# Optimization experiments

Measured on AMD Instinct MI355X. Metric: run time of the kernel, lower is better.

The kernel has to match this reference:

```python
import jax, jax.numpy as jnp
import numpy as np

B, N, M, C = 8, 2048, 2048, 512


def setup_inputs() -> dict:
    key = jax.random.key(0)
    ks = jax.random.split(key, 10)
    s = 1.0 / np.sqrt(C)
    dec_embed = jax.random.normal(ks[0], (B, N, C), dtype=jnp.float32)
    enc_embed = jax.random.normal(ks[1], (B, M, C), dtype=jnp.float32)
    trans_mat = (jax.random.uniform(ks[2], (B, N, M)) < 0.5).astype(jnp.float32)
    Wv = jax.random.uniform(ks[3], (C, C), minval=-s, maxval=s, dtype=jnp.float32)
    bv = jax.random.uniform(ks[4], (C,), minval=-s, maxval=s, dtype=jnp.float32)
    W1 = jax.random.uniform(ks[5], (C, C), minval=-s, maxval=s, dtype=jnp.float32)
    b1 = jax.random.uniform(ks[6], (C,), minval=-s, maxval=s, dtype=jnp.float32)
    W2 = jax.random.uniform(ks[7], (C, C), minval=-s, maxval=s, dtype=jnp.float32)
    b2 = jax.random.uniform(ks[8], (C,), minval=-s, maxval=s, dtype=jnp.float32)
    return {"dec_embed": dec_embed, "enc_embed": enc_embed, "trans_mat": trans_mat,
            "Wv": Wv, "bv": bv, "W1": W1, "b1": b1, "W2": W2, "b2": b2}


def reference(dec_embed, enc_embed, trans_mat, Wv, bv, W1, b1, W2, b2):
    # scores [B,N,M], elementwise-masked by trans_mat
    attn = jnp.einsum('bnc,bmc->bnm', dec_embed, enc_embed) * trans_mat
    # NONSTANDARD masked softmax: zeros participate in softmax (exp(0)=1 in denom),
    # then positions where attn==0 are re-zeroed.
    sm = jax.nn.softmax(attn, axis=-1)
    attn = jnp.where(attn != 0, sm, jnp.zeros((), attn.dtype))
    v = enc_embed @ Wv + bv                      # [B,M,C]
    v = jnp.tanh(jnp.einsum('bnm,bmc->bnc', attn, v))  # [B,N,C]
    g = dec_embed * v + dec_embed                # tanh-gate + residual
    h = jax.nn.relu(g @ W1 + b1)                 # Mlp fc1 + ReLU (drop=0)
    return h @ W2 + b2                           # Mlp fc2
```

## Files before the change

kernel.cpp:

```cpp
#include <hip/hip_runtime.h>
#include <math.h>

#define Bb 8
#define Nn 2048
#define Mm 2048
#define Cc 512

typedef __attribute__((ext_vector_type(8))) _Float16 hfrag;
typedef __attribute__((ext_vector_type(4))) float f4;
typedef __attribute__((ext_vector_type(4))) _Float16 h4;

__device__ __forceinline__ void gld16(const void* g, void* l) {
    __builtin_amdgcn_global_load_lds(
        (const __attribute__((address_space(1))) void*)g,
        (__attribute__((address_space(3))) void*)l, 16, 0, 0);
}

template<int N> __device__ __forceinline__ void wait_vmcnt() {
    if constexpr (N == 0)      asm volatile("s_waitcnt vmcnt(0)" ::: "memory");
    else if constexpr (N == 3) asm volatile("s_waitcnt vmcnt(3)" ::: "memory");
    else if constexpr (N == 4) asm volatile("s_waitcnt vmcnt(4)" ::: "memory");
    __builtin_amdgcn_sched_barrier(0);
}

template<int EPI, int BN, int SWZ>
__global__ __launch_bounds__(256) void gemm_mfma(
    const _Float16* __restrict__ Ah, long sA, int lda,
    const _Float16* __restrict__ Bh, long sB, int ldb,
    const float* __restrict__ aux, long sAux, int ldaux,
    const _Float16* __restrict__ aux2,
    float* __restrict__ mlal,
    void* __restrict__ Cout, long sC, int ldc, int K, int GX)
{
    constexpr int NI  = (BN == 128) ? 4 : 2;
    constexpr int ASL = 512;
    constexpr int BSL = BN * 4;
    constexpr int NQ  = (ASL + BSL) / 256;

    __shared__ _Float16 As[3][128 * 32];
    __shared__ _Float16 Bs[3][BN * 32];
    __shared__ _Float16 AlS[(EPI == 2) ? 32 * 128 : 4];

    int bx, by, bz;
    if (SWZ == 1) {
        const int id = blockIdx.x;
        bz = id & 7; bx = (id >> 3) % GX; by = (id >> 3) / GX;
    } else if (SWZ == 2) {
        const int id = blockIdx.x;
        bz = 0; bx = (id >> 3) % GX; by = (id & 7) + 8 * ((id >> 3) / GX);
    } else {
        bx = blockIdx.x; by = blockIdx.y; bz = 0;
    }

    const _Float16* A0 = Ah + (size_t)bz * sA;
    const _Float16* B0 = Bh + (size_t)bz * sB;

    const int tid  = threadIdx.x;
    const int wv   = tid >> 6;
    const int ln   = tid & 63;
    const int wx   = (BN == 128) ? (wv & 1) : 0;
    const int wy   = (BN == 128) ? (wv >> 1) : wv;
    const int lcol = ln & 15, quad = ln >> 4;
    const int row0w = wy * (NI * 16);
    const int col0w = wx * 64;

    const int rowBase = by * 128;
    const int colBase = bx * BN;

    const int soff = (quad ^ ((lcol >> 1) & 3)) * 8;

    f4 acc[NI][4];
    const f4 z4 = {0.f, 0.f, 0.f, 0.f};
    #pragma unroll
    for (int i = 0; i < NI; ++i)
        #pragma unroll
        for (int j = 0; j < 4; ++j) acc[i][j] = z4;

    if (EPI == 2) {
        const float* alb = mlal + (size_t)bz * (2048 * 32);
        #pragma unroll
        for (int q = 0; q < 16; ++q) {
            const int idx = q * 256 + tid;
            const int col = idx >> 5, tt = idx & 31;
            AlS[tt * 128 + col] = (_Float16)alb[(size_t)(colBase + col) * 32 + tt];
        }
        asm volatile("s_waitcnt lgkmcnt(0)" ::: "memory");
        __builtin_amdgcn_sched_barrier(0);
    }
    _Float16 als[4] = {(_Float16)0.f, (_Float16)0.f, (_Float16)0.f, (_Float16)0.f};

    auto STAGE = [&](int k0, int p) {
        #pragma unroll
        for (int q = 0; q < NQ; ++q) {
            const int c = q * 256 + wv * 64 + ln;
            if (c < ASL) {
                const int r = c >> 2;
                const int g = (c & 3) ^ ((c >> 3) & 3);
                gld16(A0 + (size_t)(rowBase + r) * lda + k0 + g * 8, &As[p][c * 8]);
            } else {
                const int cb = c - ASL;
                const int r  = cb >> 2;
                const int g  = (cb & 3) ^ ((cb >> 3) & 3);
                gld16(B0 + (size_t)(colBase + r) * ldb + k0 + g * 8, &Bs[p][cb * 8]);
            }
        }
    };

    const int NT = K >> 5;
    STAGE(0, 0);
    STAGE(32, 1);
    wait_vmcnt<NQ>();
    __builtin_amdgcn_s_barrier();

    int p = 0, pn2 = 2;
    for (int t = 0; t < NT; ++t) {
        if (t + 2 < NT) STAGE((t + 2) * 32, pn2);

        if (EPI == 2 && (t & 1) == 0) {
            const int tt = t >> 1;
            #pragma unroll
            for (int j = 0; j < 4; ++j)
                als[j] = AlS[tt * 128 + col0w + j * 16 + lcol];
        }

        hfrag af[NI], bf_[4];
        #pragma unroll
        for (int i = 0; i < NI; ++i)
            af[i]  = *(const hfrag*)&As[p][(row0w + i * 16 + lcol) * 32 + soff];
        #pragma unroll
        for (int j = 0; j < 4; ++j)
            bf_[j] = *(const hfrag*)&Bs[p][(col0w + j * 16 + lcol) * 32 + soff];

        if (EPI == 2) {
            #pragma unroll
            for (int j = 0; j < 4; ++j) bf_[j] = bf_[j] * als[j];
        }

        #pragma unroll
        for (int i = 0; i < NI; ++i)
            #pragma unroll
            for (int j = 0; j < 4; ++j)
                acc[i][j] = __builtin_amdgcn_mfma_f32_16x16x32_f16(af[i], bf_[j], acc[i][j], 0, 0, 0);

        if (t + 1 < NT) {
            if (t + 2 < NT) wait_vmcnt<NQ>();
            else            wait_vmcnt<0>();
            __builtin_amdgcn_s_barrier();
        }
        p   = (p   == 2) ? 0 : p + 1;
        pn2 = (pn2 == 2) ? 0 : pn2 + 1;
    }

    const int crow0 = rowBase + row0w + quad * 4;
    const int ccol0 = colBase + col0w + lcol;

    if (EPI == 0) {
        _Float16* E = (_Float16*)Cout + (size_t)bz * sC;
        const float* Mk = aux + (size_t)bz * sAux;
        const int t = (rowBase + row0w) >> 6;

        f4 mkA[NI], mkB[NI];
        #pragma unroll
        for (int i = 0; i < NI; ++i)
            mkA[i] = *(const f4*)(Mk + (size_t)ccol0 * ldaux + crow0 + i * 16);
        #pragma unroll
        for (int i = 0; i < NI; ++i)
            mkB[i] = *(const f4*)(Mk + (size_t)(ccol0 + 16) * ldaux + crow0 + i * 16);

        #pragma unroll
        for (int j = 0; j < 4; ++j) {
            const int n = ccol0 + j * 16;
            f4 mkN[NI];
            if (j < 2) {
                #pragma unroll
                for (int i = 0; i < NI; ++i)
                    mkN[i] = *(const f4*)(Mk + (size_t)(n + 32) * ldaux + crow0 + i * 16);
            }
            #pragma unroll
            for (int i = 0; i < NI; ++i)
                #pragma unroll
                for (int r = 0; r < 4; ++r) acc[i][j][r] *= mkA[i][r];

            float mx = acc[0][j][0];
            #pragma unroll
            for (int i = 0; i < NI; ++i)
                #pragma unroll
                for (int r = 0; r < 4; ++r) mx = fmaxf(mx, acc[i][j][r]);
            mx = fmaxf(mx, __shfl_xor(mx, 16, 64));
            mx = fmaxf(mx, __shfl_xor(mx, 32, 64));
            float l0 = 0.f;
            #pragma unroll
            for (int i = 0; i < NI; ++i) {
                h4 ev;
                #pragma unroll
                for (int r = 0; r < 4; ++r) {
                    const float s = acc[i][j][r];
                    const float e = __expf(s - mx);
                    l0 += e;
                    ev[r] = (s == 0.f) ? (_Float16)0.f : (_Float16)e;
                }
                *(h4*)(E + (size_t)n * ldc + crow0 + i * 16) = ev;
            }
            l0 += __shfl_xor(l0, 16, 64);
            l0 += __shfl_xor(l0, 32, 64);
            if (quad == 0) {
                float2 pq; pq.x = mx; pq.y = l0;
                ((float2*)mlal)[((size_t)bz * 2048 + n) * 32 + t] = pq;
            }
            #pragma unroll
            for (int i = 0; i < NI; ++i) { mkA[i] = mkB[i]; }
            if (j < 2) {
                #pragma unroll
                for (int i = 0; i < NI; ++i) mkB[i] = mkN[i];
            }
        }
    } else if (EPI == 1) {
        _Float16* C = (_Float16*)Cout;
        #pragma unroll
        for (int j = 0; j < 4; ++j) {
            const int col = ccol0 + j * 16;
            const float bi = aux[col];
            #pragma unroll
            for (int i = 0; i < NI; ++i) {
                const int rowb = crow0 + i * 16;
                const int bb = rowb >> 11, ml = rowb & 2047;
                h4 st;
                #pragma unroll
                for (int r = 0; r < 4; ++r) st[r] = (_Float16)(acc[i][j][r] + bi);
                *(h4*)(C + (size_t)bb * ((size_t)Cc * Mm) + (size_t)col * Mm + ml) = st;
            }
        }
    } else if (EPI == 2) {
        _Float16* C = (_Float16*)Cout + (size_t)bz * sC;
        const _Float16* Dg = aux2 + (size_t)bz * sC;
        #pragma unroll
        for (int i = 0; i < NI; ++i) {
            const int c0 = crow0 + i * 16;
            #pragma unroll
            for (int j = 0; j < 4; ++j) {
                const int n = ccol0 + j * 16;
                const h4 dv = *(const h4*)(Dg + (size_t)n * ldc + c0);
                h4 gv;
                #pragma unroll
                for (int r = 0; r < 4; ++r) {
                    const float a = acc[i][j][r];
                    const float th = 1.f - 2.f / (__expf(2.f * a) + 1.f);
                    gv[r] = (_Float16)((float)dv[r] * (1.f + th));
                }
                *(h4*)(C + (size_t)n * ldc + c0) = gv;
            }
        }
    } else if (EPI == 3) {
        _Float16* C = (_Float16*)Cout;
        #pragma unroll
        for (int i = 0; i < NI; ++i) {
            const int c0 = crow0 + i * 16;
            const f4 bi = *(const f4*)(aux + c0);
            #pragma unroll
            for (int j = 0; j < 4; ++j) {
                const int n = ccol0 + j * 16;
                h4 hv;
                #pragma unroll
                for (int r = 0; r < 4; ++r)
                    hv[r] = (_Float16)fmaxf(acc[i][j][r] + bi[r], 0.f);
                *(h4*)(C + (size_t)n * ldc + c0) = hv;
            }
        }
    } else {
        float* C = (float*)Cout;
        #pragma unroll
        for (int i = 0; i < NI; ++i) {
            const int c0 = crow0 + i * 16;
            const f4 bi = *(const f4*)(aux + c0);
            #pragma unroll
            for (int j = 0; j < 4; ++j) {
                const int n = ccol0 + j * 16;
                f4 ov;
                #pragma unroll
                for (int r = 0; r < 4; ++r) ov[r] = acc[i][j][r] + bi[r];
                *(f4*)(C + (size_t)n * ldc + c0) = ov;
            }
        }
    }
}

__global__ __launch_bounds__(64) void combine_kernel(
    const float* __restrict__ mlq, float* __restrict__ alpha)
{
    const int row = blockIdx.x * 64 + threadIdx.x;
    const float2* ml = (const float2*)mlq + (size_t)row * 32;
    float mt[32], lt[32];
    float m = -1e30f;
    #pragma unroll
    for (int t = 0; t < 32; ++t) {
        float2 p = ml[t];
        mt[t] = p.x; lt[t] = p.y;
        m = fmaxf(m, p.x);
    }
    float et[32], l = 0.f;
    #pragma unroll
    for (int t = 0; t < 32; ++t) {
        et[t] = __expf(mt[t] - m);
        l += lt[t] * et[t];
    }
    const float inv = 1.f / l;
    float* ap = alpha + (size_t)row * 32;
    #pragma unroll
    for (int t = 0; t < 32; ++t) ap[t] = et[t] * inv;
}

__global__ __launch_bounds__(256) void sconv(const float* __restrict__ x,
                                             _Float16* __restrict__ o)
{
    const size_t i = (size_t)blockIdx.x * 256 + threadIdx.x;
    f4 v = ((const f4*)x)[i];
    h4 hh;
    #pragma unroll
    for (int k = 0; k < 4; ++k) hh[k] = (_Float16)v[k];
    ((h4*)o)[i] = hh;
}

__global__ __launch_bounds__(256) void wconv(const float* s0, const float* s1, const float* s2,
                                             _Float16* d0, _Float16* d1, _Float16* d2)
{
    const float* Sm = blockIdx.z == 0 ? s0 : blockIdx.z == 1 ? s1 : s2;
    _Float16* D = blockIdx.z == 0 ? d0 : blockIdx.z == 1 ? d1 : d2;
    __shared__ float t[32][33];
    const int x = threadIdx.x & 31, y = threadIdx.x >> 5;
    const int gx = blockIdx.x * 32, gy = blockIdx.y * 32;
    #pragma unroll
    for (int yy = y; yy < 32; yy += 8)
        t[yy][x] = Sm[(size_t)(gy + yy) * 512 + gx + x];
    __syncthreads();
    #pragma unroll
    for (int yy = y; yy < 32; yy += 8)
        D[(size_t)(gx + yy) * 512 + gy + x] = (_Float16)t[x][yy];
}

extern "C" void kernel_launch(void* const* d_in, const int* in_sizes, int n_in,
                              void* d_out, int out_size, void* d_ws, size_t ws_size,
                              hipStream_t stream)
{
    const float* dec   = (const float*)d_in[0];
    const float* enc   = (const float*)d_in[1];
    const float* trans = (const float*)d_in[2];
    const float* Wv = (const float*)d_in[3];
    const float* bv = (const float*)d_in[4];
    const float* W1 = (const float*)d_in[5];
    const float* b1 = (const float*)d_in[6];
    const float* W2 = (const float*)d_in[7];
    const float* b2 = (const float*)d_in[8];

    char* ws = (char*)d_ws;
    _Float16* e     = (_Float16*)ws;
    float*    mlq   = (float*)(ws + 0x4000000);
    float*    alpha = (float*)(ws + 0x4400000);
    _Float16* dec_h = (_Float16*)(ws + 0x4600000);
    _Float16* Wvt   = (_Float16*)(ws + 0x5600000);
    _Float16* W1t   = Wvt + 262144;
    _Float16* W2t   = Wvt + 524288;
    _Float16* vT    = (_Float16*)(ws + 0x5800000);
    _Float16* g     = (_Float16*)(ws + 0x6800000);
    _Float16* h     = (_Float16*)(ws + 0x7800000);
    _Float16* enc_h = (_Float16*)d_out;

    sconv<<<dim3(8192), 256, 0, stream>>>(dec, dec_h);
    sconv<<<dim3(8192), 256, 0, stream>>>(enc, enc_h);
    wconv<<<dim3(16, 16, 3), 256, 0, stream>>>(Wv, W1, W2, Wvt, W1t, W2t);

    gemm_mfma<0, 128, 1><<<dim3(2048), 256, 0, stream>>>(
        enc_h, (long)Mm * Cc, 512,
        dec_h, (long)Nn * Cc, 512,
        trans, (long)Nn * Mm, 2048, nullptr, mlq,
        e, (long)Nn * Mm, 2048, 512, 16);

    combine_kernel<<<dim3(256), 64, 0, stream>>>(mlq, alpha);

    gemm_mfma<1, 64, 2><<<dim3(1024), 256, 0, stream>>>(
        enc_h, 0, 512, Wvt, 0, 512, bv, 0, 0, nullptr, nullptr,
        vT, 0, 0, 512, 8);

    gemm_mfma<2, 128, 1><<<dim3(512), 256, 0, stream>>>(
        vT, (long)Cc * Mm, 2048,
        e, (long)Nn * Mm, 2048,
        nullptr, 0, 512, dec_h, alpha,
        g, (long)Nn * Cc, 512, 2048, 16);

    gemm_mfma<3, 64, 0><<<dim3(256, 4), 256, 0, stream>>>(
        W1t, 0, 512, g, 0, 512, b1, 0, 0, nullptr, nullptr,
        h, 0, 512, 512, 0);

    gemm_mfma<4, 64, 0><<<dim3(256, 4), 256, 0, stream>>>(
        W2t, 0, 512, h, 0, 512, b2, 0, 0, nullptr, nullptr,
        d_out, 0, 512, 512, 0);
}
```

Measured before the change: 444.8 us.

## Use dedicated 256x256-tile, 512-thread kernel for masked score GEMM

Replaces the score GEMM (EPI 0 of the generic kernel, 128x128 tiles with 256 threads) with a dedicated kernel using 256x256 tiles, 8 waves, and 8x4 MFMA accumulators per wave. Larger tiles double operand reuse from LDS and cut global load traffic per FLOP. The masked-softmax epilogue still writes per-64-row partial max/sum entries so the combine step is unchanged. In exchange it uses much more LDS (96KB triple-buffered) and registers, giving lower occupancy and only 512 blocks.

```diff
diff --git a/kernel.cpp b/kernel.cpp
--- a/kernel.cpp
+++ b/kernel.cpp
@@ -21,6 +21,153 @@
     else if constexpr (N == 3) asm volatile("s_waitcnt vmcnt(3)" ::: "memory");
     else if constexpr (N == 4) asm volatile("s_waitcnt vmcnt(4)" ::: "memory");
     __builtin_amdgcn_sched_barrier(0);
+}
+
+__global__ __launch_bounds__(512) void score256(
+    const _Float16* __restrict__ Ah, long sA, int lda,
+    const _Float16* __restrict__ Bh, long sB, int ldb,
+    const float* __restrict__ Mk0, long sAux, int ldaux,
+    float* __restrict__ mlq,
+    _Float16* __restrict__ E, long sC, int ldc, int K, int GX)
+{
+    constexpr int NQ = 4;
+    __shared__ _Float16 As[3][256 * 32];
+    __shared__ _Float16 Bs[3][256 * 32];
+
+    const int id = blockIdx.x;
+    const int bz = id & 7;
+    const int bx = (id >> 3) % GX;
+    const int by = (id >> 3) / GX;
+
+    const _Float16* A0 = Ah + (size_t)bz * sA;
+    const _Float16* B0 = Bh + (size_t)bz * sB;
+
+    const int tid  = threadIdx.x;
+    const int wv   = tid >> 6;
+    const int ln   = tid & 63;
+    const int lcol = ln & 15, quad = ln >> 4;
+    const int row0w = (wv >> 2) * 128;
+    const int col0w = (wv & 3) * 64;
+    const int rowBase = by * 256;
+    const int colBase = bx * 256;
+    const int soff = (quad ^ ((lcol >> 1) & 3)) * 8;
+
+    f4 acc[8][4];
+    const f4 z4 = {0.f, 0.f, 0.f, 0.f};
+    #pragma unroll
+    for (int i = 0; i < 8; ++i)
+        #pragma unroll
+        for (int j = 0; j < 4; ++j) acc[i][j] = z4;
+
+    auto STAGE = [&](int k0, int p) {
+        #pragma unroll
+        for (int q = 0; q < 4; ++q) {
+            const int c = q * 512 + tid;
+            if (c < 1024) {
+                const int r = c >> 2;
+                const int g = (c & 3) ^ ((c >> 3) & 3);
+                gld16(A0 + (size_t)(rowBase + r) * lda + k0 + g * 8, &As[p][c * 8]);
+            } else {
+                const int cb = c - 1024;
+                const int r  = cb >> 2;
+                const int g  = (cb & 3) ^ ((cb >> 3) & 3);
+                gld16(B0 + (size_t)(colBase + r) * ldb + k0 + g * 8, &Bs[p][cb * 8]);
+            }
+        }
+    };
+
+    const int NT = K >> 5;
+    STAGE(0, 0);
+    STAGE(32, 1);
+    wait_vmcnt<NQ>();
+    __builtin_amdgcn_s_barrier();
+
+    int p = 0, pn2 = 2;
+    for (int t = 0; t < NT; ++t) {
+        if (t + 2 < NT) STAGE((t + 2) * 32, pn2);
+
+        hfrag af[8], bf_[4];
+        #pragma unroll
+        for (int i = 0; i < 8; ++i)
+            af[i]  = *(const hfrag*)&As[p][(row0w + i * 16 + lcol) * 32 + soff];
+        #pragma unroll
+        for (int j = 0; j < 4; ++j)
+            bf_[j] = *(const hfrag*)&Bs[p][(col0w + j * 16 + lcol) * 32 + soff];
+
+        #pragma unroll
+        for (int i = 0; i < 8; ++i)
+            #pragma unroll
+            for (int j = 0; j < 4; ++j)
+                acc[i][j] = __builtin_amdgcn_mfma_f32_16x16x32_f16(af[i], bf_[j], acc[i][j], 0, 0, 0);
+
+        if (t + 1 < NT) {
+            if (t + 2 < NT) wait_vmcnt<NQ>();
+            else            wait_vmcnt<0>();
+            __builtin_amdgcn_s_barrier();
+        }
+        p   = (p   == 2) ? 0 : p + 1;
+        pn2 = (pn2 == 2) ? 0 : pn2 + 1;
+    }
+
+    const int crow0 = rowBase + row0w + quad * 4;
+    const int ccol0 = colBase + col0w + lcol;
+    const int t0 = (rowBase + row0w) >> 6;
+    _Float16* Eb = E + (size_t)bz * sC;
+    const float* Mk = Mk0 + (size_t)bz * sAux;
+
+    f4 mk[8], mkN[8];
+    #pragma unroll
+    for (int i = 0; i < 8; ++i)
+        mk[i] = *(const f4*)(Mk + (size_t)ccol0 * ldaux + crow0 + i * 16);
+
+    #pragma unroll
+    for (int j = 0; j < 4; ++j) {
+        const int n = ccol0 + j * 16;
+        if (j < 3) {
+            #pragma unroll
+            for (int i = 0; i < 8; ++i)
+                mkN[i] = *(const f4*)(Mk + (size_t)(n + 16) * ldaux + crow0 + i * 16);
+        }
+        #pragma unroll
+        for (int i = 0; i < 8; ++i)
+            #pragma unroll
+            for (int r = 0; r < 4; ++r) acc[i][j][r] *= mk[i][r];
+
+        #pragma unroll
+        for (int cch = 0; cch < 2; ++cch) {
+            const int ib = cch * 4;
+            float mx = acc[ib][j][0];
+            #pragma unroll
+            for (int i = 0; i < 4; ++i)
+                #pragma unroll
+                for (int r = 0; r < 4; ++r) mx = fmaxf(mx, acc[ib + i][j][r]);
+            mx = fmaxf(mx, __shfl_xor(mx, 16, 64));
+            mx = fmaxf(mx, __shfl_xor(mx, 32, 64));
+            float l0 = 0.f;
+            #pragma unroll
+            for (int i = 0; i < 4; ++i) {
+                h4 ev;
+                #pragma unroll
+                for (int r = 0; r < 4; ++r) {
+                    const float s = acc[ib + i][j][r];
+                    const float e = __expf(s - mx);
+                    l0 += e;
+                    ev[r] = (s == 0.f) ? (_Float16)0.f : (_Float16)e;
+                }
+                *(h4*)(Eb + (size_t)n * ldc + crow0 + (ib + i) * 16) = ev;
+            }
+            l0 += __shfl_xor(l0, 16, 64);
+            l0 += __shfl_xor(l0, 32, 64);
+            if (quad == 0) {
+                float2 pq; pq.x = mx; pq.y = l0;
+                ((float2*)mlq)[((size_t)bz * 2048 + n) * 32 + t0 + cch] = pq;
+            }
+        }
+        if (j < 3) {
+            #pragma unroll
+            for (int i = 0; i < 8; ++i) mk[i] = mkN[i];
+        }
+    }
 }
 
 template<int EPI, int BN, int SWZ>
@@ -154,67 +301,7 @@
     const int crow0 = rowBase + row0w + quad * 4;
     const int ccol0 = colBase + col0w + lcol;
 
-    if (EPI == 0) {
-        _Float16* E = (_Float16*)Cout + (size_t)bz * sC;
-        const float* Mk = aux + (size_t)bz * sAux;
-        const int t = (rowBase + row0w) >> 6;
-
-        f4 mkA[NI], mkB[NI];
-        #pragma unroll
-        for (int i = 0; i < NI; ++i)
-            mkA[i] = *(const f4*)(Mk + (size_t)ccol0 * ldaux + crow0 + i * 16);
-        #pragma unroll
-        for (int i = 0; i < NI; ++i)
-            mkB[i] = *(const f4*)(Mk + (size_t)(ccol0 + 16) * ldaux + crow0 + i * 16);
-
-        #pragma unroll
-        for (int j = 0; j < 4; ++j) {
-            const int n = ccol0 + j * 16;
-            f4 mkN[NI];
-            if (j < 2) {
-                #pragma unroll
-                for (int i = 0; i < NI; ++i)
-                    mkN[i] = *(const f4*)(Mk + (size_t)(n + 32) * ldaux + crow0 + i * 16);
-            }
-            #pragma unroll
-            for (int i = 0; i < NI; ++i)
-                #pragma unroll
-                for (int r = 0; r < 4; ++r) acc[i][j][r] *= mkA[i][r];
-
-            float mx = acc[0][j][0];
-            #pragma unroll
-            for (int i = 0; i < NI; ++i)
-                #pragma unroll
-                for (int r = 0; r < 4; ++r) mx = fmaxf(mx, acc[i][j][r]);
-            mx = fmaxf(mx, __shfl_xor(mx, 16, 64));
-            mx = fmaxf(mx, __shfl_xor(mx, 32, 64));
-            float l0 = 0.f;
-            #pragma unroll
-            for (int i = 0; i < NI; ++i) {
-                h4 ev;
-                #pragma unroll
-                for (int r = 0; r < 4; ++r) {
-                    const float s = acc[i][j][r];
-                    const float e = __expf(s - mx);
-                    l0 += e;
-                    ev[r] = (s == 0.f) ? (_Float16)0.f : (_Float16)e;
-                }
-                *(h4*)(E + (size_t)n * ldc + crow0 + i * 16) = ev;
-            }
-            l0 += __shfl_xor(l0, 16, 64);
-            l0 += __shfl_xor(l0, 32, 64);
-            if (quad == 0) {
-                float2 pq; pq.x = mx; pq.y = l0;
-                ((float2*)mlal)[((size_t)bz * 2048 + n) * 32 + t] = pq;
-            }
-            #pragma unroll
-            for (int i = 0; i < NI; ++i) { mkA[i] = mkB[i]; }
-            if (j < 2) {
-                #pragma unroll
-                for (int i = 0; i < NI; ++i) mkB[i] = mkN[i];
-            }
-        }
-    } else if (EPI == 1) {
+    if (EPI == 1) {
         _Float16* C = (_Float16*)Cout;
         #pragma unroll
         for (int j = 0; j < 4; ++j) {
@@ -368,11 +455,11 @@
     sconv<<<dim3(8192), 256, 0, stream>>>(enc, enc_h);
     wconv<<<dim3(16, 16, 3), 256, 0, stream>>>(Wv, W1, W2, Wvt, W1t, W2t);
 
-    gemm_mfma<0, 128, 1><<<dim3(2048), 256, 0, stream>>>(
+    score256<<<dim3(512), 512, 0, stream>>>(
         enc_h, (long)Mm * Cc, 512,
         dec_h, (long)Nn * Cc, 512,
-        trans, (long)Nn * Mm, 2048, nullptr, mlq,
-        e, (long)Nn * Mm, 2048, 512, 16);
+        trans, (long)Nn * Mm, 2048, mlq,
+        e, (long)Nn * Mm, 2048, 512, 8);
 
     combine_kernel<<<dim3(256), 64, 0, stream>>>(mlq, alpha);
 
```

Measured after the change: 439.6 us. Within noise of the previous version (-1.2%).

## Fuse masked-score, softmax and PV GEMM into one flash-style attention kernel

Applied to the files above, without the earlier changes.

Replaces the score GEMM with its masked-exp epilogue, the combine kernel and the alpha-scaled PV GEMM with a single kernel. The new kernel keeps a running max and sum per row over 256-wide M tiles and stages the probability tile in LDS. It then feeds that tile straight into the PV MFMAs and applies the tanh gate in the epilogue. This avoids writing and re-reading the large fp16 score matrix and the per-tile max/sum buffers, and drops two launches. In exchange it runs one 256-thread block per CU with heavy LDS use, several barriers per tile and only double buffering, so latency may be poorly hidden.

```diff
diff --git a/kernel.cpp b/kernel.cpp
--- a/kernel.cpp
+++ b/kernel.cpp
@@ -23,13 +23,222 @@
     __builtin_amdgcn_sched_barrier(0);
 }
 
+__global__ __launch_bounds__(256, 1) void attn_fused(
+    const _Float16* __restrict__ Eg,
+    const _Float16* __restrict__ Qg,
+    const _Float16* __restrict__ Vg,
+    const float*    __restrict__ Mg,
+    _Float16* __restrict__ Gg)
+{
+    __shared__ _Float16 EA[2][256 * 32];
+    __shared__ _Float16 QB[2][64 * 32];
+    __shared__ _Float16 VA[2][512 * 32];
+    __shared__ _Float16 PL[64 * 256];
+    __shared__ float MXS[4][64];
+    __shared__ float LSS[4][64];
+
+    const int id = blockIdx.x;
+    const int bz = id & 7;
+    const int n0 = (id >> 3) * 64;
+
+    const _Float16* E0 = Eg + (size_t)bz * ((size_t)Mm * Cc);
+    const _Float16* Q0 = Qg + (size_t)bz * ((size_t)Nn * Cc) + (size_t)n0 * Cc;
+    const _Float16* V0 = Vg + (size_t)bz * ((size_t)Cc * Mm);
+    const float*    M0 = Mg + (size_t)bz * ((size_t)Nn * Mm);
+
+    const int tid = threadIdx.x;
+    const int wv = tid >> 6, ln = tid & 63;
+    const int lcol = ln & 15, quad = ln >> 4;
+    const int soff = (quad ^ ((lcol >> 1) & 3)) * 8;
+    char* PLb = (char*)PL;
+
+    f4 o[8][4];
+    const f4 z4 = {0.f, 0.f, 0.f, 0.f};
+    #pragma unroll
+    for (int i = 0; i < 8; ++i)
+        #pragma unroll
+        for (int j = 0; j < 4; ++j) o[i][j] = z4;
+    float mrun[4] = {0.f, 0.f, 0.f, 0.f};
+    float lrun[4] = {0.f, 0.f, 0.f, 0.f};
+
+    for (int mt = 0; mt < 8; ++mt) {
+        const int m0 = mt * 256;
+
+        f4 sa[4][4];
+        #pragma unroll
+        for (int i = 0; i < 4; ++i)
+            #pragma unroll
+            for (int j = 0; j < 4; ++j) sa[i][j] = z4;
+
+        auto SSTAGE = [&](int k0, int p) {
+            #pragma unroll
+            for (int q = 0; q < 5; ++q) {
+                const int c = q * 256 + tid;
+                if (c < 1024) {
+                    const int r = c >> 2, gsw = (c & 3) ^ ((c >> 3) & 3);
+                    gld16(E0 + (size_t)(m0 + r) * Cc + k0 + gsw * 8, &EA[p][c * 8]);
+                } else {
+                    const int cb = c - 1024;
+                    const int r = cb >> 2, gsw = (cb & 3) ^ ((cb >> 3) & 3);
+                    gld16(Q0 + (size_t)r * Cc + k0 + gsw * 8, &QB[p][cb * 8]);
+                }
+            }
+        };
+        const float* Mkb = M0 + (size_t)(n0 + lcol) * Mm + m0 + wv * 64 + quad * 4;
+        f4 mk[4], mkN[4];
+        #pragma unroll
+        for (int i = 0; i < 4; ++i) mk[i] = *(const f4*)(Mkb + i * 16);
+
+        SSTAGE(0, 0);
+        __syncthreads();
+        for (int t = 0; t < 16; ++t) {
+            const int p = t & 1;
+            if (t + 1 < 16) SSTAGE((t + 1) * 32, p ^ 1);
+            hfrag af[4], bf[4];
+            #pragma unroll
+            for (int i = 0; i < 4; ++i)
+                af[i] = *(const hfrag*)&EA[p][(wv * 64 + i * 16 + lcol) * 32 + soff];
+            #pragma unroll
+            for (int j = 0; j < 4; ++j)
+                bf[j] = *(const hfrag*)&QB[p][(j * 16 + lcol) * 32 + soff];
+            #pragma unroll
+            for (int i = 0; i < 4; ++i)
+                #pragma unroll
+                for (int j = 0; j < 4; ++j)
+                    sa[i][j] = __builtin_amdgcn_mfma_f32_16x16x32_f16(af[i], bf[j], sa[i][j], 0, 0, 0);
+            if (t + 1 < 16) __syncthreads();
+        }
+
+        #pragma unroll
+        for (int j = 0; j < 4; ++j) {
+            if (j < 3) {
+                #pragma unroll
+                for (int i = 0; i < 4; ++i)
+                    mkN[i] = *(const f4*)(Mkb + (size_t)(j + 1) * 16 * Mm + i * 16);
+            }
+            #pragma unroll
+            for (int i = 0; i < 4; ++i)
+                #pragma unroll
+                for (int r = 0; r < 4; ++r) sa[i][j][r] *= mk[i][r];
+            float mx = 0.f;
+            #pragma unroll
+            for (int i = 0; i < 4; ++i)
+                #pragma unroll
+                for (int r = 0; r < 4; ++r) mx = fmaxf(mx, sa[i][j][r]);
+            mx = fmaxf(mx, __shfl_xor(mx, 16, 64));
+            mx = fmaxf(mx, __shfl_xor(mx, 32, 64));
+            if (quad == 0) MXS[wv][j * 16 + lcol] = mx;
+            if (j < 3) {
+                #pragma unroll
+                for (int i = 0; i < 4; ++i) mk[i] = mkN[i];
+            }
+        }
+        __syncthreads();
+
+        float al[4], mnew[4];
+        #pragma unroll
+        for (int j = 0; j < 4; ++j) {
+            const int n = j * 16 + lcol;
+            float mm = mrun[j];
+            mm = fmaxf(mm, MXS[0][n]); mm = fmaxf(mm, MXS[1][n]);
+            mm = fmaxf(mm, MXS[2][n]); mm = fmaxf(mm, MXS[3][n]);
+            al[j] = __expf(mrun[j] - mm);
+            mrun[j] = mm; mnew[j] = mm;
+        }
+        #pragma unroll
+        for (int j = 0; j < 4; ++j) {
+            const int n = j * 16 + lcol;
+            float lp = 0.f;
+            #pragma unroll
+            for (int i = 0; i < 4; ++i) {
+                h4 pv;
+                #pragma unroll
+                for (int r = 0; r < 4; ++r) {
+                    const float s = sa[i][j][r];
+                    const float e = __expf(s - mnew[j]);
+                    lp += e;
+                    pv[r] = (s == 0.f) ? (_Float16)0.f : (_Float16)e;
+                }
+                *(h4*)(PLb + n * 512 +
+                       (((wv << 7) + (i << 5) + (quad << 3)) ^ ((n & 7) << 4))) = pv;
+            }
+            lp += __shfl_xor(lp, 16, 64);
+            lp += __shfl_xor(lp, 32, 64);
+            if (quad == 0) LSS[wv][n] = lp;
+        }
+        __syncthreads();
+
+        #pragma unroll
+        for (int j = 0; j < 4; ++j) {
+            const int n = j * 16 + lcol;
+            const float ls = LSS[0][n] + LSS[1][n] + LSS[2][n] + LSS[3][n];
+            lrun[j] = lrun[j] * al[j] + ls;
+            #pragma unroll
+            for (int i = 0; i < 8; ++i)
+                #pragma unroll
+                for (int r = 0; r < 4; ++r) o[i][j][r] *= al[j];
+        }
+
+        auto VSTAGE = [&](int k0, int p) {
+            #pragma unroll
+            for (int q = 0; q < 8; ++q) {
+                const int c = q * 256 + tid;
+                const int r = c >> 2, gsw = (c & 3) ^ ((c >> 3) & 3);
+                gld16(V0 + (size_t)r * Mm + m0 + k0 + gsw * 8, &VA[p][c * 8]);
+            }
+        };
+        VSTAGE(0, 0);
+        __syncthreads();
+        for (int t = 0; t < 8; ++t) {
+            const int p = t & 1;
+            if (t + 1 < 8) VSTAGE((t + 1) * 32, p ^ 1);
+            hfrag va[8], pb[4];
+            #pragma unroll
+            for (int i = 0; i < 8; ++i)
+                va[i] = *(const hfrag*)&VA[p][(wv * 128 + i * 16 + lcol) * 32 + soff];
+            #pragma unroll
+            for (int j = 0; j < 4; ++j) {
+                const int n = j * 16 + lcol;
+                pb[j] = *(const hfrag*)(PLb + n * 512 +
+                        (((t << 6) + (quad << 4)) ^ ((n & 7) << 4)));
+            }
+            #pragma unroll
+            for (int i = 0; i < 8; ++i)
+                #pragma unroll
+                for (int j = 0; j < 4; ++j)
+                    o[i][j] = __builtin_amdgcn_mfma_f32_16x16x32_f16(va[i], pb[j], o[i][j], 0, 0, 0);
+            if (t + 1 < 8) __syncthreads();
+        }
+        __syncthreads();
+    }
+
+    const _Float16* Db = Qg + (size_t)bz * ((size_t)Nn * Cc);
+    _Float16* Gb = Gg + (size_t)bz * ((size_t)Nn * Cc);
+    #pragma unroll
+    for (int j = 0; j < 4; ++j) {
+        const int n = n0 + j * 16 + lcol;
+        const float inv = 1.f / lrun[j];
+        #pragma unroll
+        for (int i = 0; i < 8; ++i) {
+            const int c0 = wv * 128 + i * 16 + quad * 4;
+            const h4 dv = *(const h4*)(Db + (size_t)n * Cc + c0);
+            h4 gv;
+            #pragma unroll
+            for (int r = 0; r < 4; ++r) {
+                const float a = o[i][j][r] * inv;
+                const float th = 1.f - 2.f / (__expf(2.f * a) + 1.f);
+                gv[r] = (_Float16)((float)dv[r] * (1.f + th));
+            }
+            *(h4*)(Gb + (size_t)n * Cc + c0) = gv;
+        }
+    }
+}
+
 template<int EPI, int BN, int SWZ>
 __global__ __launch_bounds__(256) void gemm_mfma(
     const _Float16* __restrict__ Ah, long sA, int lda,
     const _Float16* __restrict__ Bh, long sB, int ldb,
     const float* __restrict__ aux, long sAux, int ldaux,
-    const _Float16* __restrict__ aux2,
-    float* __restrict__ mlal,
     void* __restrict__ Cout, long sC, int ldc, int K, int GX)
 {
     constexpr int NI  = (BN == 128) ? 4 : 2;
@@ -39,7 +248,6 @@
 
     __shared__ _Float16 As[3][128 * 32];
     __shared__ _Float16 Bs[3][BN * 32];
-    __shared__ _Float16 AlS[(EPI == 2) ? 32 * 128 : 4];
 
     int bx, by, bz;
     if (SWZ == 1) {
@@ -66,7 +274,6 @@
 
     const int rowBase = by * 128;
     const int colBase = bx * BN;
-
     const int soff = (quad ^ ((lcol >> 1) & 3)) * 8;
 
     f4 acc[NI][4];
@@ -75,19 +282,6 @@
     for (int i = 0; i < NI; ++i)
         #pragma unroll
         for (int j = 0; j < 4; ++j) acc[i][j] = z4;
-
-    if (EPI == 2) {
-        const float* alb = mlal + (size_t)bz * (2048 * 32);
-        #pragma unroll
-        for (int q = 0; q < 16; ++q) {
-            const int idx = q * 256 + tid;
-            const int col = idx >> 5, tt = idx & 31;
-            AlS[tt * 128 + col] = (_Float16)alb[(size_t)(colBase + col) * 32 + tt];
-        }
-        asm volatile("s_waitcnt lgkmcnt(0)" ::: "memory");
-        __builtin_amdgcn_sched_barrier(0);
-    }
-    _Float16 als[4] = {(_Float16)0.f, (_Float16)0.f, (_Float16)0.f, (_Float16)0.f};
 
     auto STAGE = [&](int k0, int p) {
         #pragma unroll
@@ -116,13 +310,6 @@
     for (int t = 0; t < NT; ++t) {
         if (t + 2 < NT) STAGE((t + 2) * 32, pn2);
 
-        if (EPI == 2 && (t & 1) == 0) {
-            const int tt = t >> 1;
-            #pragma unroll
-            for (int j = 0; j < 4; ++j)
-                als[j] = AlS[tt * 128 + col0w + j * 16 + lcol];
-        }
-
         hfrag af[NI], bf_[4];
         #pragma unroll
         for (int i = 0; i < NI; ++i)
@@ -130,11 +317,6 @@
         #pragma unroll
         for (int j = 0; j < 4; ++j)
             bf_[j] = *(const hfrag*)&Bs[p][(col0w + j * 16 + lcol) * 32 + soff];
-
-        if (EPI == 2) {
-            #pragma unroll
-            for (int j = 0; j < 4; ++j) bf_[j] = bf_[j] * als[j];
-        }
 
         #pragma unroll
         for (int i = 0; i < NI; ++i)
@@ -154,67 +336,7 @@
     const int crow0 = rowBase + row0w + quad * 4;
     const int ccol0 = colBase + col0w + lcol;
 
-    if (EPI == 0) {
-        _Float16* E = (_Float16*)Cout + (size_t)bz * sC;
-        const float* Mk = aux + (size_t)bz * sAux;
-        const int t = (rowBase + row0w) >> 6;
-
-        f4 mkA[NI], mkB[NI];
-        #pragma unroll
-        for (int i = 0; i < NI; ++i)
-            mkA[i] = *(const f4*)(Mk + (size_t)ccol0 * ldaux + crow0 + i * 16);
-        #pragma unroll
-        for (int i = 0; i < NI; ++i)
-            mkB[i] = *(const f4*)(Mk + (size_t)(ccol0 + 16) * ldaux + crow0 + i * 16);
-
-        #pragma unroll
-        for (int j = 0; j < 4; ++j) {
-            const int n = ccol0 + j * 16;
-            f4 mkN[NI];
-            if (j < 2) {
-                #pragma unroll
-                for (int i = 0; i < NI; ++i)
-                    mkN[i] = *(const f4*)(Mk + (size_t)(n + 32) * ldaux + crow0 + i * 16);
-            }
-            #pragma unroll
-            for (int i = 0; i < NI; ++i)
-                #pragma unroll
-                for (int r = 0; r < 4; ++r) acc[i][j][r] *= mkA[i][r];
-
-            float mx = acc[0][j][0];
-            #pragma unroll
-            for (int i = 0; i < NI; ++i)
-                #pragma unroll
-                for (int r = 0; r < 4; ++r) mx = fmaxf(mx, acc[i][j][r]);
-            mx = fmaxf(mx, __shfl_xor(mx, 16, 64));
-            mx = fmaxf(mx, __shfl_xor(mx, 32, 64));
-            float l0 = 0.f;
-            #pragma unroll
-            for (int i = 0; i < NI; ++i) {
-                h4 ev;
-                #pragma unroll
-                for (int r = 0; r < 4; ++r) {
-                    const float s = acc[i][j][r];
-                    const float e = __expf(s - mx);
-                    l0 += e;
-                    ev[r] = (s == 0.f) ? (_Float16)0.f : (_Float16)e;
-                }
-                *(h4*)(E + (size_t)n * ldc + crow0 + i * 16) = ev;
-            }
-            l0 += __shfl_xor(l0, 16, 64);
-            l0 += __shfl_xor(l0, 32, 64);
-            if (quad == 0) {
-                float2 pq; pq.x = mx; pq.y = l0;
-                ((float2*)mlal)[((size_t)bz * 2048 + n) * 32 + t] = pq;
-            }
-            #pragma unroll
-            for (int i = 0; i < NI; ++i) { mkA[i] = mkB[i]; }
-            if (j < 2) {
-                #pragma unroll
-                for (int i = 0; i < NI; ++i) mkB[i] = mkN[i];
-            }
-        }
-    } else if (EPI == 1) {
+    if (EPI == 1) {
         _Float16* C = (_Float16*)Cout;
         #pragma unroll
         for (int j = 0; j < 4; ++j) {
@@ -230,26 +352,6 @@
                 *(h4*)(C + (size_t)bb * ((size_t)Cc * Mm) + (size_t)col * Mm + ml) = st;
             }
         }
-    } else if (EPI == 2) {
-        _Float16* C = (_Float16*)Cout + (size_t)bz * sC;
-        const _Float16* Dg = aux2 + (size_t)bz * sC;
-        #pragma unroll
-        for (int i = 0; i < NI; ++i) {
-            const int c0 = crow0 + i * 16;
-            #pragma unroll
-            for (int j = 0; j < 4; ++j) {
-                const int n = ccol0 + j * 16;
-                const h4 dv = *(const h4*)(Dg + (size_t)n * ldc + c0);
-                h4 gv;
-                #pragma unroll
-                for (int r = 0; r < 4; ++r) {
-                    const float a = acc[i][j][r];
-                    const float th = 1.f - 2.f / (__expf(2.f * a) + 1.f);
-                    gv[r] = (_Float16)((float)dv[r] * (1.f + th));
-                }
-                *(h4*)(C + (size_t)n * ldc + c0) = gv;
-            }
-        }
     } else if (EPI == 3) {
         _Float16* C = (_Float16*)Cout;
         #pragma unroll
@@ -282,31 +384,6 @@
             }
         }
     }
-}
-
-__global__ __launch_bounds__(64) void combine_kernel(
-    const float* __restrict__ mlq, float* __restrict__ alpha)
-{
-    const int row = blockIdx.x * 64 + threadIdx.x;
-    const float2* ml = (const float2*)mlq + (size_t)row * 32;
-    float mt[32], lt[32];
-    float m = -1e30f;
-    #pragma unroll
-    for (int t = 0; t < 32; ++t) {
-        float2 p = ml[t];
-        mt[t] = p.x; lt[t] = p.y;
-        m = fmaxf(m, p.x);
-    }
-    float et[32], l = 0.f;
-    #pragma unroll
-    for (int t = 0; t < 32; ++t) {
-        et[t] = __expf(mt[t] - m);
-        l += lt[t] * et[t];
-    }
-    const float inv = 1.f / l;
-    float* ap = alpha + (size_t)row * 32;
-    #pragma unroll
-    for (int t = 0; t < 32; ++t) ap[t] = et[t] * inv;
 }
 
 __global__ __launch_bounds__(256) void sconv(const float* __restrict__ x,
@@ -352,9 +429,6 @@
     const float* b2 = (const float*)d_in[8];
 
     char* ws = (char*)d_ws;
-    _Float16* e     = (_Float16*)ws;
-    float*    mlq   = (float*)(ws + 0x4000000);
-    float*    alpha = (float*)(ws + 0x4400000);
     _Float16* dec_h = (_Float16*)(ws + 0x4600000);
     _Float16* Wvt   = (_Float16*)(ws + 0x5600000);
     _Float16* W1t   = Wvt + 262144;
@@ -368,29 +442,17 @@
     sconv<<<dim3(8192), 256, 0, stream>>>(enc, enc_h);
     wconv<<<dim3(16, 16, 3), 256, 0, stream>>>(Wv, W1, W2, Wvt, W1t, W2t);
 
-    gemm_mfma<0, 128, 1><<<dim3(2048), 256, 0, stream>>>(
-        enc_h, (long)Mm * Cc, 512,
-        dec_h, (long)Nn * Cc, 512,
-        trans, (long)Nn * Mm, 2048, nullptr, mlq,
-        e, (long)Nn * Mm, 2048, 512, 16);
-
-    combine_kernel<<<dim3(256), 64, 0, stream>>>(mlq, alpha);
-
     gemm_mfma<1, 64, 2><<<dim3(1024), 256, 0, stream>>>(
-        enc_h, 0, 512, Wvt, 0, 512, bv, 0, 0, nullptr, nullptr,
+        enc_h, 0, 512, Wvt, 0, 512, bv, 0, 0,
         vT, 0, 0, 512, 8);
 
-    gemm_mfma<2, 128, 1><<<dim3(512), 256, 0, stream>>>(
-        vT, (long)Cc * Mm, 2048,
-        e, (long)Nn * Mm, 2048,
-        nullptr, 0, 512, dec_h, alpha,
-        g, (long)Nn * Cc, 512, 2048, 16);
+    attn_fused<<<dim3(256), 256, 0, stream>>>(enc_h, dec_h, vT, trans, g);
 
     gemm_mfma<3, 64, 0><<<dim3(256, 4), 256, 0, stream>>>(
-        W1t, 0, 512, g, 0, 512, b1, 0, 0, nullptr, nullptr,
+        W1t, 0, 512, g, 0, 512, b1, 0, 0,
         h, 0, 512, 512, 0);
 
     gemm_mfma<4, 64, 0><<<dim3(256, 4), 256, 0, stream>>>(
-        W2t, 0, 512, h, 0, 512, b2, 0, 0, nullptr, nullptr,
+        W2t, 0, 512, h, 0, 512, b2, 0, 0,
         d_out, 0, 512, 512, 0);
 }
```

Result: slower. 469.9 us (+5.7%).
